# Kernel optimization log

Measured on AMD Instinct MI355X. Metric: run time of the kernel, lower is better.

Reference implementation:

```python
import jax, jax.numpy as jnp
from jax import lax
import numpy as np

D_MODEL = 1024
D_STATE = 64
D_CONV = 4
EXPAND = 2
HEADDIM = 128
NGROUPS = 1
CHUNK = 256
D_INNER = EXPAND * D_MODEL            # 2048
NHEADS = D_INNER // HEADDIM           # 16
CONV_DIM = D_INNER + 2 * NGROUPS * D_STATE  # 2176
D_IN_PROJ = D_INNER + CONV_DIM + NHEADS      # 4240


def _segsum_exp(t):
    """t: (..., T) -> exp(segsum(t)): (..., T, T), lower-triangular (zeros above diag)."""
    T = t.shape[-1]
    cs = jnp.cumsum(t, axis=-1)
    d = cs[..., :, None] - cs[..., None, :]
    mask = jnp.tril(jnp.ones((T, T), dtype=bool))
    return jnp.where(mask, jnp.exp(jnp.where(mask, d, 0.0)), 0.0)


def _ssd_scan(x, dt, A, Bm, Cm, chunk):
    """Chunked SSD selective scan (Mamba2 reference math).
    x: (B,L,H,P), dt: (B,L,H), A: (H,), Bm/Cm: (B,L,G,N). Returns y: (B,L,H,P)."""
    Bz, L, H, P = x.shape
    G, N = Bm.shape[2], Bm.shape[3]
    nc = L // chunk
    # broadcast groups -> heads
    rep = H // G
    Bh = jnp.repeat(Bm, rep, axis=2)  # (B,L,H,N)
    Ch = jnp.repeat(Cm, rep, axis=2)
    # chunk
    xc = x.reshape(Bz, nc, chunk, H, P)
    dtc = dt.reshape(Bz, nc, chunk, H)
    Bc = Bh.reshape(Bz, nc, chunk, H, N)
    Cc = Ch.reshape(Bz, nc, chunk, H, N)
    dA = dtc * A[None, None, None, :]              # (B,nc,Q,H)
    dAh = jnp.transpose(dA, (0, 1, 3, 2))          # (B,nc,H,Q)
    A_cs = jnp.cumsum(dAh, axis=-1)                # (B,nc,H,Q)
    # intra-chunk (diagonal) part
    Lmat = _segsum_exp(dAh)                        # (B,nc,H,Q,Q)
    Y_diag = jnp.einsum('bcqhn,bckhn,bchqk,bckh,bckhp->bcqhp', Cc, Bc, Lmat, dtc, xc)
    # per-chunk states
    decay_states = jnp.exp(A_cs[..., -1:] - A_cs)  # (B,nc,H,Q)
    states = jnp.einsum('bckhn,bchk,bckh,bckhp->bchpn', Bc, decay_states, dtc, xc)
    # inter-chunk recurrence via segsum over chunks
    chunk_total = jnp.transpose(A_cs[..., -1], (0, 2, 1))  # (B,H,nc)
    padded = jnp.pad(chunk_total, ((0, 0), (0, 0), (1, 0)))
    decay_chunk = _segsum_exp(padded)              # (B,H,nc+1,nc+1)
    states_cat = jnp.concatenate([jnp.zeros_like(states[:, :1]), states], axis=1)
    new_states = jnp.einsum('bhzc,bchpn->bzhpn', decay_chunk, states_cat)
    prev = new_states[:, :-1]                      # state entering each chunk
    Y_off = jnp.einsum('bcqhn,bchpn,bchq->bcqhp', Cc, prev, jnp.exp(A_cs))
    return (Y_diag + Y_off).reshape(Bz, L, H, P)


def setup_inputs() -> dict:
    key = jax.random.key(0)
    ks = jax.random.split(key, 8)
    x = jax.random.normal(ks[0], (2, 4096, D_MODEL), dtype=jnp.float32)
    W_in = jax.random.normal(ks[1], (D_IN_PROJ, D_MODEL), dtype=jnp.float32) * 0.02
    conv_w = jax.random.normal(ks[2], (CONV_DIM, 1, D_CONV), dtype=jnp.float32) * 0.2
    conv_b = jnp.zeros((CONV_DIM,), dtype=jnp.float32)
    A_init = jax.random.uniform(ks[3], (NHEADS,), minval=1.0, maxval=16.0)
    A_log = jnp.log(A_init).astype(jnp.float32)
    dtv = jnp.exp(jax.random.uniform(ks[4], (NHEADS,)) * (np.log(0.1) - np.log(0.001)) + np.log(0.001))
    dtv = jnp.clip(dtv, 0.001, None)
    dt_bias = (dtv + jnp.log(-jnp.expm1(-dtv))).astype(jnp.float32)
    D_skip = jnp.ones((NHEADS,), dtype=jnp.float32)
    W_out = jax.random.normal(ks[5], (D_MODEL, D_INNER), dtype=jnp.float32) * 0.02
    return {"x": x, "W_in": W_in, "conv_w": conv_w, "conv_b": conv_b,
            "A_log": A_log, "dt_bias": dt_bias, "D_skip": D_skip, "W_out": W_out}


def reference(x, W_in, conv_w, conv_b, A_log, dt_bias, D_skip, W_out):
    Bz, L, _ = x.shape
    proj = x @ W_in.T                              # (B,L,4240)
    z = proj[..., :D_INNER]
    xBC = proj[..., D_INNER:D_INNER + CONV_DIM]
    dt_raw = proj[..., D_INNER + CONV_DIM:]
    # causal depthwise conv1d (torch pads d_conv-1 both sides then truncates to L == left-pad)
    xBC_t = jnp.transpose(xBC, (0, 2, 1))          # (B,conv_dim,L)
    conv = lax.conv_general_dilated(xBC_t, conv_w, (1,), [(D_CONV - 1, 0)],
                                    dimension_numbers=('NCH', 'OIH', 'NCH'),
                                    feature_group_count=CONV_DIM)
    xBC = jnp.transpose(conv + conv_b[None, :, None], (0, 2, 1))
    xBC = jax.nn.silu(xBC)
    x_ssm = xBC[..., :D_INNER].reshape(Bz, L, NHEADS, HEADDIM)
    B_ssm = xBC[..., D_INNER:D_INNER + NGROUPS * D_STATE].reshape(Bz, L, NGROUPS, D_STATE)
    C_ssm = xBC[..., D_INNER + NGROUPS * D_STATE:].reshape(Bz, L, NGROUPS, D_STATE)
    dt = jax.nn.softplus(dt_raw + dt_bias[None, None, :])
    A = -jnp.exp(A_log)
    y = _ssd_scan(x_ssm, dt, A, B_ssm, C_ssm, CHUNK)
    y = y + x_ssm * D_skip[None, None, :, None]
    y = y.reshape(Bz, L, D_INNER)
    y = y * jax.nn.silu(z)                         # gated output
    return y @ W_out.T
```

## Files before the change

kernel.cpp:

```cpp
#include <hip/hip_runtime.h>

#define B_     2
#define L_     4096
#define DM     1024
#define DI     2048
#define NH     16
#define HD     128
#define NS     64
#define T_     256
#define NC     16
#define CONVD  2176
#define DPROJ  4240
#define NPADIN 4352

typedef __attribute__((ext_vector_type(8))) short bf16x8;
typedef __attribute__((ext_vector_type(4))) float f32x4;

__device__ __forceinline__ void bsplit(float x, unsigned short& h, unsigned short& l) {
    unsigned u = __float_as_uint(x);
    unsigned t = u + 0x7FFFu + ((u >> 16) & 1u);
    h = (unsigned short)(t >> 16);
    float lo = x - __uint_as_float(t & 0xFFFF0000u);
    l = (unsigned short)(__float_as_uint(lo) >> 16);
}

__global__ __launch_bounds__(256) void split_pad(
    const float* __restrict__ W, unsigned short* __restrict__ Wh,
    unsigned short* __restrict__ Wl, int srcN4, int dstN4)
{
    int i = blockIdx.x * 256 + threadIdx.x;
    if (i >= dstN4) return;
    ushort4 h = {0,0,0,0}, l = {0,0,0,0};
    if (i < srcN4) {
        float4 v = *(const float4*)(W + (size_t)i * 4);
        bsplit(v.x, h.x, l.x); bsplit(v.y, h.y, l.y);
        bsplit(v.z, h.z, l.z); bsplit(v.w, h.w, l.w);
    }
    *(ushort4*)(Wh + (size_t)i * 4) = h;
    *(ushort4*)(Wl + (size_t)i * 4) = l;
}

__global__ __launch_bounds__(256, 2) void mfma_gemm_lds(
    const unsigned short* __restrict__ Ah, const unsigned short* __restrict__ Al,
    long arow, const unsigned short* __restrict__ Wh, const unsigned short* __restrict__ Wl,
    float* __restrict__ C, int N, int K, int ldc, int nyt)
{
    __shared__ unsigned short AhL[128 * 40];
    __shared__ unsigned short AlL[128 * 40];
    __shared__ unsigned short BhL[128 * 40];
    __shared__ unsigned short BlL[128 * 40];

    int NB = gridDim.x;
    int bid = blockIdx.x;
    int t = (bid & 7) * (NB >> 3) + (bid >> 3);
    int xt = t / nyt, yt = t % nyt;
    int tid = threadIdx.x;
    int lane = tid & 63, w = tid >> 6;
    int m0 = yt * 128, n0 = xt * 128;
    int mblk = (w >> 1) * 64, nblk = (w & 1) * 64;
    int fr = lane & 15;
    int fk = (lane >> 4) * 8;

    int sr0 = tid >> 2, sc0 = (tid & 3) * 8;
    int sr1 = (tid + 256) >> 2, sc1 = ((tid + 256) & 3) * 8;

    f32x4 acc[4][4];
    #pragma unroll
    for (int i = 0; i < 4; i++)
        #pragma unroll
        for (int j = 0; j < 4; j++) acc[i][j] = (f32x4){0.f, 0.f, 0.f, 0.f};

    int nk = K >> 5;
    for (int ks = 0; ks < nk; ks++) {
        int k0 = ks << 5;
        __syncthreads();
        {
            size_t a0 = (size_t)(m0 + sr0) * arow + k0 + sc0;
            size_t a1 = (size_t)(m0 + sr1) * arow + k0 + sc1;
            size_t b0 = (size_t)(n0 + sr0) * K + k0 + sc0;
            size_t b1 = (size_t)(n0 + sr1) * K + k0 + sc1;
            *(uint4*)&AhL[sr0 * 40 + sc0] = *(const uint4*)(Ah + a0);
            *(uint4*)&AhL[sr1 * 40 + sc1] = *(const uint4*)(Ah + a1);
            *(uint4*)&AlL[sr0 * 40 + sc0] = *(const uint4*)(Al + a0);
            *(uint4*)&AlL[sr1 * 40 + sc1] = *(const uint4*)(Al + a1);
            *(uint4*)&BhL[sr0 * 40 + sc0] = *(const uint4*)(Wh + b0);
            *(uint4*)&BhL[sr1 * 40 + sc1] = *(const uint4*)(Wh + b1);
            *(uint4*)&BlL[sr0 * 40 + sc0] = *(const uint4*)(Wl + b0);
            *(uint4*)&BlL[sr1 * 40 + sc1] = *(const uint4*)(Wl + b1);
        }
        __syncthreads();

        bf16x8 ah[4], al[4], bh[4], bl[4];
        #pragma unroll
        for (int tt = 0; tt < 4; tt++) {
            ah[tt] = *(const bf16x8*)&AhL[(mblk + tt*16 + fr) * 40 + fk];
            al[tt] = *(const bf16x8*)&AlL[(mblk + tt*16 + fr) * 40 + fk];
            bh[tt] = *(const bf16x8*)&BhL[(nblk + tt*16 + fr) * 40 + fk];
            bl[tt] = *(const bf16x8*)&BlL[(nblk + tt*16 + fr) * 40 + fk];
        }
        #pragma unroll
        for (int mt = 0; mt < 4; mt++)
            #pragma unroll
            for (int nt = 0; nt < 4; nt++) {
                f32x4 a = acc[mt][nt];
                a = __builtin_amdgcn_mfma_f32_16x16x32_bf16(al[mt], bh[nt], a, 0, 0, 0);
                a = __builtin_amdgcn_mfma_f32_16x16x32_bf16(ah[mt], bl[nt], a, 0, 0, 0);
                a = __builtin_amdgcn_mfma_f32_16x16x32_bf16(ah[mt], bh[nt], a, 0, 0, 0);
                acc[mt][nt] = a;
            }
    }

    int crow = (lane >> 4) * 4;
    #pragma unroll
    for (int mt = 0; mt < 4; mt++) {
        int rbase = m0 + mblk + mt*16 + crow;
        #pragma unroll
        for (int nt = 0; nt < 4; nt++) {
            int col = n0 + nblk + nt*16 + fr;
            if (col < N) {
                #pragma unroll
                for (int i = 0; i < 4; i++)
                    C[(size_t)(rbase + i) * ldc + col] = acc[mt][nt][i];
            }
        }
    }
}

__global__ void conv_silu(const float* __restrict__ proj, const float* __restrict__ w,
                          const float* __restrict__ bias, float* __restrict__ xbc)
{
    size_t idx = (size_t)blockIdx.x * 256 + threadIdx.x;
    if (idx >= (size_t)L_ * CONVD) return;
    int c = (int)(idx % CONVD);
    int l = (int)(idx / CONVD);
    float acc = bias[c];
    #pragma unroll
    for (int j = 0; j < 4; j++) {
        int ll = l - 3 + j;
        if (ll >= 0)
            acc = fmaf(proj[(size_t)ll * DPROJ + DI + c], w[c*4+j], acc);
    }
    acc = acc / (1.f + expf(-acc));
    xbc[(size_t)l * CONVD + c] = acc;
}

__global__ __launch_bounds__(256) void dt_scan(
    const float* __restrict__ proj, const float* __restrict__ A_log,
    const float* __restrict__ dt_bias, float* __restrict__ dt_t, float* __restrict__ acs)
{
    int blk = blockIdx.x;
    int h = blk % NH;
    int c = blk / NH;
    int t = threadIdx.x;
    size_t row = (size_t)(c * T_ + t);
    float raw = proj[row * DPROJ + DI + CONVD + h] + dt_bias[h];
    float dtv = (raw > 20.f) ? raw : log1pf(expf(raw));
    float Ah = -expf(A_log[h]);
    __shared__ float buf[T_];
    buf[t] = dtv * Ah;
    __syncthreads();
    for (int off = 1; off < T_; off <<= 1) {
        float add = (t >= off) ? buf[t - off] : 0.f;
        __syncthreads();
        buf[t] += add;
        __syncthreads();
    }
    size_t o = (size_t)blk * T_ + t;
    dt_t[o] = dtv;
    acs[o]  = buf[t];
}

__global__ __launch_bounds__(256) void chunk_states(
    const float* __restrict__ xbc, const float* __restrict__ dt_t,
    const float* __restrict__ acs, float* __restrict__ states)
{
    int bid = blockIdx.x;
    int blk = (bid & 7) * 32 + (bid >> 3);
    int h = blk % NH;
    int c = blk / NH;
    int tid = threadIdx.x;
    __shared__ float coef[T_];
    __shared__ __align__(16) float xs[32][HD];
    __shared__ float Bs[32][NS + 1];
    {
        size_t o = (size_t)blk * T_;
        float last = acs[o + T_ - 1];
        coef[tid] = expf(last - acs[o + tid]) * dt_t[o + tid];
    }
    __syncthreads();
    int tx = tid % 16;
    int ty = tid / 16;
    float acc[8][4];
    #pragma unroll
    for (int i = 0; i < 8; i++)
        #pragma unroll
        for (int j = 0; j < 4; j++) acc[i][j] = 0.f;
    size_t rowbase = (size_t)(c * T_);
    for (int t0 = 0; t0 < T_; t0 += 32) {
        #pragma unroll
        for (int i = 0; i < 4; i++) {
            int idx = tid + 256 * i;
            int r = idx >> 5, cv = idx & 31;
            float4 v = *(const float4*)(xbc + (rowbase + t0 + r) * CONVD + h * HD + cv * 4);
            *(float4*)&xs[r][cv * 4] = v;
        }
        #pragma unroll
        for (int i = 0; i < 2; i++) {
            int idx = tid + 256 * i;
            int r = idx >> 4, cv = idx & 15;
            float4 v = *(const float4*)(xbc + (rowbase + t0 + r) * CONVD + DI + cv * 4);
            float wc = coef[t0 + r];
            Bs[r][cv*4+0] = v.x * wc; Bs[r][cv*4+1] = v.y * wc;
            Bs[r][cv*4+2] = v.z * wc; Bs[r][cv*4+3] = v.w * wc;
        }
        __syncthreads();
        #pragma unroll
        for (int tt = 0; tt < 32; tt++) {
            float xv[8], bv[4];
            #pragma unroll
            for (int i = 0; i < 8; i++) xv[i] = xs[tt][ty*8+i];
            #pragma unroll
            for (int j = 0; j < 4; j++) bv[j] = Bs[tt][tx*4+j];
            #pragma unroll
            for (int i = 0; i < 8; i++)
                #pragma unroll
                for (int j = 0; j < 4; j++)
                    acc[i][j] = fmaf(xv[i], bv[j], acc[i][j]);
        }
        __syncthreads();
    }
    size_t base = (size_t)blk * HD * NS;
    #pragma unroll
    for (int i = 0; i < 8; i++)
        #pragma unroll
        for (int j = 0; j < 4; j++)
            states[base + (size_t)(ty*8+i) * NS + tx*4+j] = acc[i][j];
}

__global__ __launch_bounds__(256) void prev_rec(
    float* __restrict__ states, const float* __restrict__ acs)
{
    int blk = blockIdx.x;
    int pq = blk % 4;
    int h = blk / 4;
    int tid = threadIdx.x;
    int s = tid * 8;
    int p = pq * 32 + s / NS;
    int n0 = s % NS;
    float run[8];
    #pragma unroll
    for (int j = 0; j < 8; j++) run[j] = 0.f;
    for (int c = 0; c < NC; c++) {
        size_t ch = (size_t)(c * NH + h);
        size_t off = ch * HD * NS + (size_t)p * NS + n0;
        float sv[8];
        #pragma unroll
        for (int j = 0; j < 8; j++) sv[j] = states[off + j];
        #pragma unroll
        for (int j = 0; j < 8; j++) states[off + j] = run[j];
        float f = expf(acs[ch * T_ + T_ - 1]);
        #pragma unroll
        for (int j = 0; j < 8; j++) run[j] = sv[j] + f * run[j];
    }
}

__global__ __launch_bounds__(512, 2) void y_chunk(
    const float* __restrict__ xbc, const float* __restrict__ dt_t,
    const float* __restrict__ acs, const float* __restrict__ prev,
    const float* __restrict__ D_skip, float* zy )
{
    int bid = blockIdx.x;
    int l = (bid & 7) * 32 + (bid >> 3);
    int h = l & 15;
    int c = l >> 4;
    int tid = threadIdx.x;

    __shared__ __align__(16) float smem[18496];
    float* H     = smem;
    float* Cs    = smem + 8320;
    float* Bsh   = smem + 10496;
    float* xs    = smem + 12672;
    float* Ss    = smem + 16896;
    float* acs_s = smem + 17952;
    float* dts   = smem + 18208;
    float* coefs = smem + 18464;

    size_t bch = (size_t)(c * NH + h);
    size_t rowbase = (size_t)(c * T_);
    if (tid < 256) {
        acs_s[tid] = acs[bch * T_ + tid];
        dts[tid]   = dt_t[bch * T_ + tid];
    }

    float4 pB, pC, pX0, pX1;
    int rBC = tid >> 4, cBC = (tid & 15) * 4;
    int rX0 = tid >> 5, cX0 = (tid & 31) * 4;
    int rX1 = (tid + 512) >> 5;
    auto issue = [&](int s) {
        const float* base = xbc + (rowbase + s * 32) * CONVD;
        pB  = *(const float4*)(base + (size_t)rBC * CONVD + DI + cBC);
        pC  = *(const float4*)(base + (size_t)rBC * CONVD + DI + NS + cBC);
        pX0 = *(const float4*)(base + (size_t)rX0 * CONVD + h * HD + cX0);
        pX1 = *(const float4*)(base + (size_t)rX1 * CONVD + h * HD + cX0);
    };
    issue(0);

    int pp = tid >> 2, n0 = (tid & 3) * 16;
    {
        const float* src = prev + bch * (HD * NS) + (size_t)pp * NS + n0;
        #pragma unroll
        for (int j4 = 0; j4 < 4; j4++) {
            float4 v = *(const float4*)(src + j4 * 4);
            H[pp*65 + n0 + j4*4 + 0] = v.x;
            H[pp*65 + n0 + j4*4 + 1] = v.y;
            H[pp*65 + n0 + j4*4 + 2] = v.z;
            H[pp*65 + n0 + j4*4 + 3] = v.w;
        }
    }
    __syncthreads();

    float Dh = D_skip[h];
    int q2 = tid & 15;
    int p4 = (tid >> 4) * 4;
    int kq = tid >> 4;
    int kk0 = tid & 15;

    for (int s = 0; s < 8; s++) {
        int b32 = s * 32;
        float base = (s == 0) ? 0.f : acs_s[b32 - 1];
        float aL = acs_s[b32 + 31];

        *(float4*)&Bsh[rBC * 68 + cBC]  = pB;
        *(float4*)&Cs [rBC * 68 + cBC]  = pC;
        *(float4*)&xs [rX0 * 132 + cX0] = pX0;
        *(float4*)&xs [rX1 * 132 + cX0] = pX1;
        if (tid < 32)
            coefs[tid] = dts[b32 + tid] * expf(aL - acs_s[b32 + tid]);
        __syncthreads();

        if (s < 7) issue(s + 1);
        float4 pZ0 = *(const float4*)(zy + (rowbase + b32 + q2) * DPROJ + h * HD + p4);
        float4 pZ1 = *(const float4*)(zy + (rowbase + b32 + q2 + 16) * DPROJ + h * HD + p4);

        {
            float sv0 = 0.f, sv1 = 0.f;
            for (int n = 0; n < NS; n++) {
                float cq = Cs[kq * 68 + n];
                sv0 = fmaf(cq, Bsh[kk0 * 68 + n], sv0);
                sv1 = fmaf(cq, Bsh[(kk0 + 16) * 68 + n], sv1);
            }
            float v0 = 0.f, v1 = 0.f;
            if (kq >= kk0)
                v0 = sv0 * expf(acs_s[b32+kq] - acs_s[b32+kk0]) * dts[b32+kk0];
            if (kq >= kk0+16)
                v1 = sv1 * expf(acs_s[b32+kq] - acs_s[b32+kk0+16]) * dts[b32+kk0+16];
            Ss[kq * 33 + kk0]      = v0;
            Ss[kq * 33 + kk0 + 16] = v1;
        }
        __syncthreads();

        {
            float a00=0.f,a01=0.f,a02=0.f,a03=0.f;
            float a10=0.f,a11=0.f,a12=0.f,a13=0.f;
            for (int kk = 0; kk < 32; kk++) {
                float s0 = Ss[q2 * 33 + kk];
                float s1 = Ss[(q2+16) * 33 + kk];
                float x0 = xs[kk*132 + p4 + 0];
                float x1 = xs[kk*132 + p4 + 1];
                float x2 = xs[kk*132 + p4 + 2];
                float x3 = xs[kk*132 + p4 + 3];
                a00 = fmaf(s0,x0,a00); a01 = fmaf(s0,x1,a01);
                a02 = fmaf(s0,x2,a02); a03 = fmaf(s0,x3,a03);
                a10 = fmaf(s1,x0,a10); a11 = fmaf(s1,x1,a11);
                a12 = fmaf(s1,x2,a12); a13 = fmaf(s1,x3,a13);
            }
            float eq0 = expf(acs_s[b32 + q2] - base);
            float eq1 = expf(acs_s[b32 + q2 + 16] - base);
            for (int n = 0; n < NS; n++) {
                float c0 = Cs[q2*68 + n] * eq0;
                float c1 = Cs[(q2+16)*68 + n] * eq1;
                float h0 = H[(p4+0)*65 + n];
                float h1 = H[(p4+1)*65 + n];
                float h2 = H[(p4+2)*65 + n];
                float h3 = H[(p4+3)*65 + n];
                a00 = fmaf(c0,h0,a00); a01 = fmaf(c0,h1,a01);
                a02 = fmaf(c0,h2,a02); a03 = fmaf(c0,h3,a03);
                a10 = fmaf(c1,h0,a10); a11 = fmaf(c1,h1,a11);
                a12 = fmaf(c1,h2,a12); a13 = fmaf(c1,h3,a13);
            }
            float y00 = (a00 + Dh * xs[q2*132 + p4+0]) * (pZ0.x / (1.f + expf(-pZ0.x)));
            float y01 = (a01 + Dh * xs[q2*132 + p4+1]) * (pZ0.y / (1.f + expf(-pZ0.y)));
            float y02 = (a02 + Dh * xs[q2*132 + p4+2]) * (pZ0.z / (1.f + expf(-pZ0.z)));
            float y03 = (a03 + Dh * xs[q2*132 + p4+3]) * (pZ0.w / (1.f + expf(-pZ0.w)));
            float y10 = (a10 + Dh * xs[(q2+16)*132 + p4+0]) * (pZ1.x / (1.f + expf(-pZ1.x)));
            float y11 = (a11 + Dh * xs[(q2+16)*132 + p4+1]) * (pZ1.y / (1.f + expf(-pZ1.y)));
            float y12 = (a12 + Dh * xs[(q2+16)*132 + p4+2]) * (pZ1.z / (1.f + expf(-pZ1.z)));
            float y13 = (a13 + Dh * xs[(q2+16)*132 + p4+3]) * (pZ1.w / (1.f + expf(-pZ1.w)));
            unsigned short* yb0 = (unsigned short*)(zy + (rowbase + b32 + q2) * DPROJ + DI);
            unsigned short* yb1 = (unsigned short*)(zy + (rowbase + b32 + q2 + 16) * DPROJ + DI);
            ushort4 h4, l4;
            bsplit(y00, h4.x, l4.x); bsplit(y01, h4.y, l4.y);
            bsplit(y02, h4.z, l4.z); bsplit(y03, h4.w, l4.w);
            *(ushort4*)(yb0 + h * HD + p4)        = h4;
            *(ushort4*)(yb0 + 2048 + h * HD + p4) = l4;
            bsplit(y10, h4.x, l4.x); bsplit(y11, h4.y, l4.y);
            bsplit(y12, h4.z, l4.z); bsplit(y13, h4.w, l4.w);
            *(ushort4*)(yb1 + h * HD + p4)        = h4;
            *(ushort4*)(yb1 + 2048 + h * HD + p4) = l4;
        }
        __syncthreads();

        {
            float decay = expf(aL - base);
            float hreg[16];
            #pragma unroll
            for (int j = 0; j < 16; j++)
                hreg[j] = H[pp*65 + n0 + j] * decay;
            for (int t = 0; t < 32; t++) {
                float xa = xs[t*132 + pp] * coefs[t];
                #pragma unroll
                for (int j = 0; j < 16; j++)
                    hreg[j] = fmaf(xa, Bsh[t*68 + n0 + j], hreg[j]);
            }
            #pragma unroll
            for (int j = 0; j < 16; j++)
                H[pp*65 + n0 + j] = hreg[j];
        }
        __syncthreads();
    }
}

extern "C" void kernel_launch(void* const* d_in, const int* in_sizes, int n_in,
                              void* d_out, int out_size, void* d_ws, size_t ws_size,
                              hipStream_t stream)
{
    const float* x       = (const float*)d_in[0];
    const float* W_in    = (const float*)d_in[1];
    const float* conv_w  = (const float*)d_in[2];
    const float* conv_b  = (const float*)d_in[3];
    const float* A_log   = (const float*)d_in[4];
    const float* dt_bias = (const float*)d_in[5];
    const float* D_skip  = (const float*)d_in[6];
    const float* W_out   = (const float*)d_in[7];
    float* out = (float*)d_out;

    float* proj   = (float*)d_ws;
    float* xbc    = proj   + (size_t)L_ * DPROJ;
    float* dt_t   = xbc    + (size_t)L_ * CONVD;
    float* acs    = dt_t   + (size_t)NC * NH * T_;
    float* states = acs    + (size_t)NC * NH * T_;
    unsigned short* WinH  = (unsigned short*)(states + (size_t)NC * NH * HD * NS);
    unsigned short* WinL  = WinH  + (size_t)NPADIN * DM;
    unsigned short* WoutH = WinL  + (size_t)NPADIN * DM;
    unsigned short* WoutL = WoutH + (size_t)DM * DI;
    unsigned short* XH = (unsigned short*)xbc;
    unsigned short* XL = XH + (size_t)L_ * DM;
    unsigned short* projU = (unsigned short*)proj;

    dim3 blk(256);
    {
        int s4in = (DPROJ * DM) / 4, d4in = (NPADIN * DM) / 4;
        split_pad<<<dim3((d4in + 255) / 256), blk, 0, stream>>>(W_in, WinH, WinL, s4in, d4in);
        int n4out = (DM * DI) / 4;
        split_pad<<<dim3((n4out + 255) / 256), blk, 0, stream>>>(W_out, WoutH, WoutL, n4out, n4out);
    }

    for (int b = 0; b < B_; b++) {
        const float* xb = x + (size_t)b * L_ * DM;
        float* outb = out + (size_t)b * L_ * DM;
        int x4 = (L_ * DM) / 4;
        split_pad<<<dim3((x4 + 255) / 256), blk, 0, stream>>>(xb, XH, XL, x4, x4);
        mfma_gemm_lds<<<dim3((NPADIN / 128) * (L_ / 128)), blk, 0, stream>>>(
            XH, XL, (long)DM, WinH, WinL, proj, DPROJ, DM, DPROJ, L_ / 128);
        conv_silu<<<dim3((unsigned)(((size_t)L_ * CONVD + 255) / 256)), blk, 0, stream>>>(
            proj, conv_w, conv_b, xbc);
        dt_scan<<<dim3(NC * NH), blk, 0, stream>>>(proj, A_log, dt_bias, dt_t, acs);
        chunk_states<<<dim3(NC * NH), blk, 0, stream>>>(xbc, dt_t, acs, states);
        prev_rec<<<dim3(NH * 4), blk, 0, stream>>>(states, acs);
        y_chunk<<<dim3(NC * NH), dim3(512), 0, stream>>>(xbc, dt_t, acs, states, D_skip, proj);
        mfma_gemm_lds<<<dim3((DM / 128) * (L_ / 128)), blk, 0, stream>>>(
            projU + (size_t)DI * 2, projU + (size_t)DI * 2 + 2048, (long)(DPROJ * 2),
            WoutH, WoutL, outb, DM, DI, DM, L_ / 128);
    }
}
```

Measured before the change: 790.6 us.

## Split y_chunk across headdim halves and raise occupancy bounds

The y_chunk kernel now splits each (chunk, head) block into two blocks, each handling half of the 128 head-dim columns. This doubles the grid from 256 to 512 blocks and shrinks shared memory per block, so more blocks can be resident and the GPU is better filled. The cost is that the C·B score matrix and its exp-decay weights are computed twice per head, and each thread produces fewer outputs. Launch bounds minimum-blocks hints are also raised to 4 for the GEMM and y_chunk, which may force the compiler to use fewer registers and risks spilling.

```diff
diff --git a/kernel.cpp b/kernel.cpp
--- a/kernel.cpp
+++ b/kernel.cpp
@@ -40,7 +40,7 @@
     *(ushort4*)(Wl + (size_t)i * 4) = l;
 }
 
-__global__ __launch_bounds__(256, 2) void mfma_gemm_lds(
+__global__ __launch_bounds__(256, 4) void mfma_gemm_lds(
     const unsigned short* __restrict__ Ah, const unsigned short* __restrict__ Al,
     long arow, const unsigned short* __restrict__ Wh, const unsigned short* __restrict__ Wl,
     float* __restrict__ C, int N, int K, int ldc, int nyt)
@@ -264,26 +264,29 @@
     }
 }
 
-__global__ __launch_bounds__(512, 2) void y_chunk(
+__global__ __launch_bounds__(512, 4) void y_chunk(
     const float* __restrict__ xbc, const float* __restrict__ dt_t,
     const float* __restrict__ acs, const float* __restrict__ prev,
     const float* __restrict__ D_skip, float* zy )
 {
     int bid = blockIdx.x;
-    int l = (bid & 7) * 32 + (bid >> 3);
-    int h = l & 15;
-    int c = l >> 4;
+    int l = (bid & 7) * 64 + (bid >> 3);
+    int ph = l & 1;
+    int ch = l >> 1;
+    int h = ch & 15;
+    int c = ch >> 4;
     int tid = threadIdx.x;
-
-    __shared__ __align__(16) float smem[18496];
+    int pbase = ph * 64;
+
+    __shared__ __align__(16) float smem[12288];
     float* H     = smem;
-    float* Cs    = smem + 8320;
-    float* Bsh   = smem + 10496;
-    float* xs    = smem + 12672;
-    float* Ss    = smem + 16896;
-    float* acs_s = smem + 17952;
-    float* dts   = smem + 18208;
-    float* coefs = smem + 18464;
+    float* Cs    = smem + 4160;
+    float* Bsh   = smem + 6336;
+    float* xs    = smem + 8512;
+    float* Ss    = smem + 10688;
+    float* acs_s = smem + 11744;
+    float* dts   = smem + 12000;
+    float* coefs = smem + 12256;
 
     size_t bch = (size_t)(c * NH + h);
     size_t rowbase = (size_t)(c * T_);
@@ -292,36 +295,33 @@
         dts[tid]   = dt_t[bch * T_ + tid];
     }
 
-    float4 pB, pC, pX0, pX1;
+    float4 pB, pC, pX;
     int rBC = tid >> 4, cBC = (tid & 15) * 4;
-    int rX0 = tid >> 5, cX0 = (tid & 31) * 4;
-    int rX1 = (tid + 512) >> 5;
     auto issue = [&](int s) {
         const float* base = xbc + (rowbase + s * 32) * CONVD;
-        pB  = *(const float4*)(base + (size_t)rBC * CONVD + DI + cBC);
-        pC  = *(const float4*)(base + (size_t)rBC * CONVD + DI + NS + cBC);
-        pX0 = *(const float4*)(base + (size_t)rX0 * CONVD + h * HD + cX0);
-        pX1 = *(const float4*)(base + (size_t)rX1 * CONVD + h * HD + cX0);
+        pB = *(const float4*)(base + (size_t)rBC * CONVD + DI + cBC);
+        pC = *(const float4*)(base + (size_t)rBC * CONVD + DI + NS + cBC);
+        pX = *(const float4*)(base + (size_t)rBC * CONVD + h * HD + pbase + cBC);
     };
     issue(0);
 
-    int pp = tid >> 2, n0 = (tid & 3) * 16;
+    int pp = tid >> 3, n8 = (tid & 7) * 8;
     {
-        const float* src = prev + bch * (HD * NS) + (size_t)pp * NS + n0;
-        #pragma unroll
-        for (int j4 = 0; j4 < 4; j4++) {
+        const float* src = prev + bch * (HD * NS) + (size_t)(pbase + pp) * NS + n8;
+        #pragma unroll
+        for (int j4 = 0; j4 < 2; j4++) {
             float4 v = *(const float4*)(src + j4 * 4);
-            H[pp*65 + n0 + j4*4 + 0] = v.x;
-            H[pp*65 + n0 + j4*4 + 1] = v.y;
-            H[pp*65 + n0 + j4*4 + 2] = v.z;
-            H[pp*65 + n0 + j4*4 + 3] = v.w;
+            H[pp*65 + n8 + j4*4 + 0] = v.x;
+            H[pp*65 + n8 + j4*4 + 1] = v.y;
+            H[pp*65 + n8 + j4*4 + 2] = v.z;
+            H[pp*65 + n8 + j4*4 + 3] = v.w;
         }
     }
     __syncthreads();
 
     float Dh = D_skip[h];
     int q2 = tid & 15;
-    int p4 = (tid >> 4) * 4;
+    int p2 = (tid >> 4) * 2;
     int kq = tid >> 4;
     int kk0 = tid & 15;
 
@@ -330,17 +330,16 @@
         float base = (s == 0) ? 0.f : acs_s[b32 - 1];
         float aL = acs_s[b32 + 31];
 
-        *(float4*)&Bsh[rBC * 68 + cBC]  = pB;
-        *(float4*)&Cs [rBC * 68 + cBC]  = pC;
-        *(float4*)&xs [rX0 * 132 + cX0] = pX0;
-        *(float4*)&xs [rX1 * 132 + cX0] = pX1;
+        *(float4*)&Bsh[rBC * 68 + cBC] = pB;
+        *(float4*)&Cs [rBC * 68 + cBC] = pC;
+        *(float4*)&xs [rBC * 68 + cBC] = pX;
         if (tid < 32)
             coefs[tid] = dts[b32 + tid] * expf(aL - acs_s[b32 + tid]);
         __syncthreads();
 
         if (s < 7) issue(s + 1);
-        float4 pZ0 = *(const float4*)(zy + (rowbase + b32 + q2) * DPROJ + h * HD + p4);
-        float4 pZ1 = *(const float4*)(zy + (rowbase + b32 + q2 + 16) * DPROJ + h * HD + p4);
+        float2 pZ0 = *(const float2*)(zy + (rowbase + b32 + q2) * DPROJ + h * HD + pbase + p2);
+        float2 pZ1 = *(const float2*)(zy + (rowbase + b32 + q2 + 16) * DPROJ + h * HD + pbase + p2);
 
         {
             float sv0 = 0.f, sv1 = 0.f;
@@ -360,71 +359,56 @@
         __syncthreads();
 
         {
-            float a00=0.f,a01=0.f,a02=0.f,a03=0.f;
-            float a10=0.f,a11=0.f,a12=0.f,a13=0.f;
+            float a00=0.f,a01=0.f,a10=0.f,a11=0.f;
             for (int kk = 0; kk < 32; kk++) {
                 float s0 = Ss[q2 * 33 + kk];
                 float s1 = Ss[(q2+16) * 33 + kk];
-                float x0 = xs[kk*132 + p4 + 0];
-                float x1 = xs[kk*132 + p4 + 1];
-                float x2 = xs[kk*132 + p4 + 2];
-                float x3 = xs[kk*132 + p4 + 3];
+                float x0 = xs[kk*68 + p2 + 0];
+                float x1 = xs[kk*68 + p2 + 1];
                 a00 = fmaf(s0,x0,a00); a01 = fmaf(s0,x1,a01);
-                a02 = fmaf(s0,x2,a02); a03 = fmaf(s0,x3,a03);
                 a10 = fmaf(s1,x0,a10); a11 = fmaf(s1,x1,a11);
-                a12 = fmaf(s1,x2,a12); a13 = fmaf(s1,x3,a13);
             }
             float eq0 = expf(acs_s[b32 + q2] - base);
             float eq1 = expf(acs_s[b32 + q2 + 16] - base);
             for (int n = 0; n < NS; n++) {
                 float c0 = Cs[q2*68 + n] * eq0;
                 float c1 = Cs[(q2+16)*68 + n] * eq1;
-                float h0 = H[(p4+0)*65 + n];
-                float h1 = H[(p4+1)*65 + n];
-                float h2 = H[(p4+2)*65 + n];
-                float h3 = H[(p4+3)*65 + n];
+                float h0 = H[(p2+0)*65 + n];
+                float h1 = H[(p2+1)*65 + n];
                 a00 = fmaf(c0,h0,a00); a01 = fmaf(c0,h1,a01);
-                a02 = fmaf(c0,h2,a02); a03 = fmaf(c0,h3,a03);
                 a10 = fmaf(c1,h0,a10); a11 = fmaf(c1,h1,a11);
-                a12 = fmaf(c1,h2,a12); a13 = fmaf(c1,h3,a13);
-            }
-            float y00 = (a00 + Dh * xs[q2*132 + p4+0]) * (pZ0.x / (1.f + expf(-pZ0.x)));
-            float y01 = (a01 + Dh * xs[q2*132 + p4+1]) * (pZ0.y / (1.f + expf(-pZ0.y)));
-            float y02 = (a02 + Dh * xs[q2*132 + p4+2]) * (pZ0.z / (1.f + expf(-pZ0.z)));
-            float y03 = (a03 + Dh * xs[q2*132 + p4+3]) * (pZ0.w / (1.f + expf(-pZ0.w)));
-            float y10 = (a10 + Dh * xs[(q2+16)*132 + p4+0]) * (pZ1.x / (1.f + expf(-pZ1.x)));
-            float y11 = (a11 + Dh * xs[(q2+16)*132 + p4+1]) * (pZ1.y / (1.f + expf(-pZ1.y)));
-            float y12 = (a12 + Dh * xs[(q2+16)*132 + p4+2]) * (pZ1.z / (1.f + expf(-pZ1.z)));
-            float y13 = (a13 + Dh * xs[(q2+16)*132 + p4+3]) * (pZ1.w / (1.f + expf(-pZ1.w)));
+            }
+            float y00 = (a00 + Dh * xs[q2*68 + p2+0]) * (pZ0.x / (1.f + expf(-pZ0.x)));
+            float y01 = (a01 + Dh * xs[q2*68 + p2+1]) * (pZ0.y / (1.f + expf(-pZ0.y)));
+            float y10 = (a10 + Dh * xs[(q2+16)*68 + p2+0]) * (pZ1.x / (1.f + expf(-pZ1.x)));
+            float y11 = (a11 + Dh * xs[(q2+16)*68 + p2+1]) * (pZ1.y / (1.f + expf(-pZ1.y)));
             unsigned short* yb0 = (unsigned short*)(zy + (rowbase + b32 + q2) * DPROJ + DI);
             unsigned short* yb1 = (unsigned short*)(zy + (rowbase + b32 + q2 + 16) * DPROJ + DI);
-            ushort4 h4, l4;
-            bsplit(y00, h4.x, l4.x); bsplit(y01, h4.y, l4.y);
-            bsplit(y02, h4.z, l4.z); bsplit(y03, h4.w, l4.w);
-            *(ushort4*)(yb0 + h * HD + p4)        = h4;
-            *(ushort4*)(yb0 + 2048 + h * HD + p4) = l4;
-            bsplit(y10, h4.x, l4.x); bsplit(y11, h4.y, l4.y);
-            bsplit(y12, h4.z, l4.z); bsplit(y13, h4.w, l4.w);
-            *(ushort4*)(yb1 + h * HD + p4)        = h4;
-            *(ushort4*)(yb1 + 2048 + h * HD + p4) = l4;
+            ushort2 h2v, l2v;
+            bsplit(y00, h2v.x, l2v.x); bsplit(y01, h2v.y, l2v.y);
+            *(ushort2*)(yb0 + h * HD + pbase + p2)        = h2v;
+            *(ushort2*)(yb0 + 2048 + h * HD + pbase + p2) = l2v;
+            bsplit(y10, h2v.x, l2v.x); bsplit(y11, h2v.y, l2v.y);
+            *(ushort2*)(yb1 + h * HD + pbase + p2)        = h2v;
+            *(ushort2*)(yb1 + 2048 + h * HD + pbase + p2) = l2v;
         }
         __syncthreads();
 
         {
             float decay = expf(aL - base);
-            float hreg[16];
-            #pragma unroll
-            for (int j = 0; j < 16; j++)
-                hreg[j] = H[pp*65 + n0 + j] * decay;
+            float hreg[8];
+            #pragma unroll
+            for (int j = 0; j < 8; j++)
+                hreg[j] = H[pp*65 + n8 + j] * decay;
             for (int t = 0; t < 32; t++) {
-                float xa = xs[t*132 + pp] * coefs[t];
+                float xa = xs[t*68 + pp] * coefs[t];
                 #pragma unroll
-                for (int j = 0; j < 16; j++)
-                    hreg[j] = fmaf(xa, Bsh[t*68 + n0 + j], hreg[j]);
-            }
-            #pragma unroll
-            for (int j = 0; j < 16; j++)
-                H[pp*65 + n0 + j] = hreg[j];
+                for (int j = 0; j < 8; j++)
+                    hreg[j] = fmaf(xa, Bsh[t*68 + n8 + j], hreg[j]);
+            }
+            #pragma unroll
+            for (int j = 0; j < 8; j++)
+                H[pp*65 + n8 + j] = hreg[j];
         }
         __syncthreads();
     }
@@ -477,7 +461,7 @@
         dt_scan<<<dim3(NC * NH), blk, 0, stream>>>(proj, A_log, dt_bias, dt_t, acs);
         chunk_states<<<dim3(NC * NH), blk, 0, stream>>>(xbc, dt_t, acs, states);
         prev_rec<<<dim3(NH * 4), blk, 0, stream>>>(states, acs);
-        y_chunk<<<dim3(NC * NH), dim3(512), 0, stream>>>(xbc, dt_t, acs, states, D_skip, proj);
+        y_chunk<<<dim3(NC * NH * 2), dim3(512), 0, stream>>>(xbc, dt_t, acs, states, D_skip, proj);
         mfma_gemm_lds<<<dim3((DM / 128) * (L_ / 128)), blk, 0, stream>>>(
             projU + (size_t)DI * 2, projU + (size_t)DI * 2 + 2048, (long)(DPROJ * 2),
             WoutH, WoutL, outb, DM, DI, DM, L_ / 128);
```

Measured after the change: 1.159 ms. +46.5%, slower.
